# Optimization experiments

Measured on AMD Instinct MI355X. Metric: run time of the kernel, lower is better.

The kernel has to match this reference:

```python
import jax, jax.numpy as jnp
import numpy as np
from jax import lax

# dims (match init_kwargs / input_specs)
B, CIN, H, W = 32, 32, 48, 160
CL = 32            # out_lstm (per-direction hidden channels)
CO = 64            # out_channels of conv
KH, KW, STRIDE = 2, 2, 2
EPS = 1e-5         # BatchNorm2d eps


def setup_inputs() -> dict:
    key = jax.random.key(0)
    ks = jax.random.split(key, 9)
    s = 0.1
    return {
        "x": jax.random.normal(ks[0], (B, CIN, H, W), jnp.float32),
        # per-direction MDLSTM weights: input proj, left-hidden, top-hidden, bias
        "Wx": jax.random.normal(ks[1], (4, CIN, 5 * CL), jnp.float32) * s,
        "Ul": jax.random.normal(ks[2], (4, CL, 5 * CL), jnp.float32) * s,
        "Ut": jax.random.normal(ks[3], (4, CL, 5 * CL), jnp.float32) * s,
        "bias": jnp.zeros((4, 5 * CL), jnp.float32),
        # conv_0 (the original forward uses conv_0 for all four directions)
        "conv_w": jax.random.normal(ks[4], (CO, CL, KH, KW), jnp.float32) * s,
        "conv_b": jnp.zeros((CO,), jnp.float32),
        # BatchNorm2d affine params (training-mode batch statistics)
        "gamma": jnp.ones((CO,), jnp.float32),
        "beta": jnp.zeros((CO,), jnp.float32),
    }


def _mdlstm_dir(xz, Ul, Ut):
    """One scan direction of a Graves-style 2D MDLSTM.
    xz: [H, W, B, 5C] precomputed input projection (incl. bias).
    Gates order: i, f_left, f_top, o, g. Returns h: [H, W, B, C]."""
    C = Ul.shape[0]
    Bn = xz.shape[2]
    zero_row = jnp.zeros((xz.shape[1], Bn, C), xz.dtype)  # [W, B, C]

    def col_step(carry, inp):
        h_l, c_l = carry                 # [B, C] state from the left
        z_c, h_t, c_t = inp              # per-cell input proj + top state
        z = z_c + h_l @ Ul + h_t @ Ut    # [B, 5C]
        i, fl, ft, o, g = jnp.split(z, 5, axis=-1)
        c = (jax.nn.sigmoid(fl) * c_l + jax.nn.sigmoid(ft) * c_t
             + jax.nn.sigmoid(i) * jnp.tanh(g))
        h = jax.nn.sigmoid(o) * jnp.tanh(c)
        return (h, c), (h, c)

    def row_step(carry, xz_row):
        h_top, c_top = carry             # [W, B, C] previous row states
        init = (jnp.zeros((Bn, C), xz.dtype), jnp.zeros((Bn, C), xz.dtype))
        _, (h_row, c_row) = lax.scan(col_step, init, (xz_row, h_top, c_top))
        return (h_row, c_row), h_row

    _, h_all = lax.scan(row_step, (zero_row, zero_row), xz)  # [H, W, B, C]
    return h_all


def reference(x, Wx, Ul, Ut, bias, conv_w, conv_b, gamma, beta):
    xh = jnp.transpose(x, (2, 3, 0, 1))  # [H, W, B, Cin]
    dirs = []
    for d in range(4):  # 4 scan directions: flip combinations of H / W
        xd = xh
        if d in (1, 3):
            xd = xd[:, ::-1]
        if d in (2, 3):
            xd = xd[::-1]
        # big upfront GEMM: input projection for every cell
        xz = jnp.einsum('hwbc,cd->hwbd', xd, Wx[d]) + bias[d]
        h = _mdlstm_dir(xz, Ul[d], Ut[d])
        if d in (2, 3):
            h = h[::-1]
        if d in (1, 3):
            h = h[:, ::-1]
        dirs.append(h)
    # original applies conv_0 to each direction then sums; conv is linear so
    # conv0(x0)+conv0(x1)+conv0(x2)+conv0(x3) == conv0(x0+x1+x2+x3) + 4*bias
    hsum = dirs[0] + dirs[1] + dirs[2] + dirs[3]           # [H, W, B, C]
    hsum = jnp.transpose(hsum, (2, 3, 0, 1))               # [B, C, H, W]
    y = lax.conv_general_dilated(hsum, conv_w, (STRIDE, STRIDE), 'VALID',
                                 dimension_numbers=('NCHW', 'OIHW', 'NCHW'))
    y = y + (4.0 * conv_b)[None, :, None, None]
    y = jnp.tanh(y)
    # BatchNorm2d, training mode (biased batch variance, eps=1e-5)
    mean = y.mean(axis=(0, 2, 3), keepdims=True)
    var = jnp.square(y - mean).mean(axis=(0, 2, 3), keepdims=True)
    yn = (y - mean) * lax.rsqrt(var + EPS)
    return gamma[None, :, None, None] * yn + beta[None, :, None, None]
```

## Files before the change

### kernel.cpp

```cpp
#include <hip/hip_runtime.h>

typedef __bf16 bf16;
typedef __bf16 bf16x8 __attribute__((ext_vector_type(8)));
typedef float  f32x4  __attribute__((ext_vector_type(4)));
typedef int    i32x2  __attribute__((ext_vector_type(2)));
typedef unsigned long long u64;

#define HH 48
#define WW 160
#define BB 32
#define CINC 32
#define CLC 32
#define COC 64
#define OHH 24
#define OWW 80
#define RD 8
#define SLOT_U64 1280

__device__ __forceinline__ bool probe_bf16(const void* gamma) {
  return ((const unsigned short*)gamma)[0] == 0x3F80;
}
__device__ __forceinline__ float rd_in(const void* p, int idx, bool isb) {
  return isb ? (float)((const bf16*)p)[idx] : ((const float*)p)[idx];
}
__device__ __forceinline__ float fsig(float x) {
  return 1.0f / (1.0f + __expf(-x));
}
__device__ __forceinline__ float ftanh(float x) {
  return 1.0f - 2.0f / (1.0f + __expf(2.0f * x));
}

union PK64 { bf16 h[4]; u64 q; };
union FRU { f32x4 f; bf16x8 v; };

__global__ __launch_bounds__(256) void k_params(const void* __restrict__ bias,
                                                const void* __restrict__ conv_w,
                                                const void* __restrict__ conv_b,
                                                const void* __restrict__ gamma,
                                                const void* __restrict__ beta,
                                                float* __restrict__ biasf,
                                                float* __restrict__ convwT,
                                                float* __restrict__ convbf,
                                                float* __restrict__ gammaf,
                                                float* __restrict__ betaf) {
  bool isb = probe_bf16(gamma);
  int i = blockIdx.x * 256 + threadIdx.x;
  if (i < 640)  biasf[i]  = rd_in(bias, i, isb);
  if (i < 8192) {
    int kk = i >> 11, co = (i >> 5) & 63, cl = i & 31;
    convwT[i] = rd_in(conv_w, co * 128 + cl * 4 + kk, isb);
  }
  if (i < 64) {
    convbf[i] = rd_in(conv_b, i, isb);
    gammaf[i] = rd_in(gamma, i, isb);
    betaf[i]  = rd_in(beta, i, isb);
  }
}

__global__ __launch_bounds__(256) void k_transpose3(const void* __restrict__ x,
                                                    const void* __restrict__ gamma,
                                                    bf16* __restrict__ xT3) {
  bool isb = probe_bf16(gamma);
  int h  = blockIdx.x / 20;
  int w0 = (blockIdx.x % 20) * 8;
  __shared__ float tile[BB * CINC * 8];
  for (int e = threadIdx.x; e < BB * CINC * 8; e += 256) {
    int dw = e & 7, c = (e >> 3) & 31, b = e >> 8;
    tile[e] = rd_in(x, ((b * CINC + c) * HH + h) * WW + w0 + dw, isb);
  }
  __syncthreads();
  const size_t PL = (size_t)HH * WW * 1024;
  for (int e = threadIdx.x; e < BB * CINC * 8; e += 256) {
    int c = e & 31, b = (e >> 5) & 31, dw = e >> 10;
    float v = tile[(b * 32 + c) * 8 + dw];
    bf16 p0 = (bf16)v; float r = v - (float)p0;
    bf16 p1 = (bf16)r;
    bf16 p2 = (bf16)(r - (float)p1);
    size_t base = ((size_t)h * WW + w0 + dw) * 1024 + b * 32 + c;
    xT3[base] = p0; xT3[PL + base] = p1; xT3[2 * PL + base] = p2;
  }
}

#define MF5(Aop, PB, KS)                                                       \
  { _Pragma("unroll") for (int g = 0; g < 5; g++)                              \
      acc[g] = __builtin_amdgcn_mfma_f32_16x16x32_bf16(Aop, Ufr[PB][KS][g],    \
                                                       acc[g], 0, 0, 0); }

__global__ __launch_bounds__(256, 1) void k_mdlstm(
    const bf16* __restrict__ xT3,
    const void* __restrict__ Wx, const void* __restrict__ Ul,
    const void* __restrict__ Ut, const void* __restrict__ gamma_raw,
    const float* __restrict__ biasf,
    u64* __restrict__ ring,
    int* __restrict__ flags,
    int* __restrict__ cons,
    float* __restrict__ planes) {
  bool isb = probe_bf16(gamma_raw);
  int d = blockIdx.x / 48, i = blockIdx.x % 48;
  int fi = d * 48 + i;
  int gh = (d & 2) ? (HH - 1 - i) : i;
  int tid = threadIdx.x;
  int lane = tid & 63, wv = tid >> 6;
  int mtile = wv & 1, hf = wv >> 1, nsub = hf * 16;
  int l15 = lane & 15, quad = lane >> 4;
  int m = mtile * 16 + l15;
  int cl  = nsub + l15;
  int b0q = mtile * 16 + quad * 4;
  int rb = lane & 3;
  int bC = b0q + rb;
  int cl0C = nsub + (l15 & 12);

  __shared__ bf16 Ust[160 * 96];
  __shared__ __align__(16) bf16 Afr[2][3][1024];

  bf16x8 Ufr[3][3][5];
  for (int q = 0; q < 3; q++) {
    for (int e = tid; e < 160 * 96; e += 256) {
      int n = e / 96, k = e % 96;
      float v;
      if (k < 32)      v = rd_in(Ul, (d * 32 + k) * 160 + n, isb);
      else if (k < 64) v = rd_in(Ut, (d * 32 + (k - 32)) * 160 + n, isb);
      else             v = rd_in(Wx, (d * 32 + (k - 64)) * 160 + n, isb);
      bf16 p0 = (bf16)v; float r = v - (float)p0;
      bf16 p1 = (bf16)r;
      Ust[e] = (q == 0) ? p0 : (q == 1) ? p1 : (bf16)(r - (float)p1);
    }
    __syncthreads();
#pragma unroll
    for (int ks = 0; ks < 3; ks++)
#pragma unroll
      for (int g = 0; g < 5; g++)
        Ufr[q][ks][g] =
            *(const bf16x8*)(&Ust[(nsub + 32 * g + l15) * 96 + ks * 32 + quad * 8]);
    __syncthreads();
  }
  float bi[5];
#pragma unroll
  for (int g = 0; g < 5; g++) bi[g] = biasf[d * 160 + 32 * g + nsub + l15];
  for (int e = tid; e < 2 * 3 * 1024; e += 256) (&Afr[0][0][0])[e] = (bf16)0.f;
  __syncthreads();

  float creg[4] = {0.f, 0.f, 0.f, 0.f};

  int fprev = (i > 0)  ? fi - 1 : fi;
  int fnext = (i < 47) ? fi + 1 : fi;
  int* fdst = flags + ((fi << 5) + (mtile << 1) + hf);
  const int* fsrc = flags + ((fprev << 5) + (mtile << 1));
  int* cdst = cons + ((fi << 5) + (mtile << 1) + hf);
  const int* csrc = cons + ((fnext << 5) + (mtile << 1));
  int flag_known = (i > 0) ? -1 : 0x7FFFFFFF;
  int cons_known = -1;
  i32x2 pf; pf.x = -1; pf.y = -1;

  const int a_rd = m * 64 + ((quad * 16) ^ ((m & 6) << 3));
  const int a_wr = bC * 64 + ((cl0C * 2) ^ ((bC & 6) << 3));

  bf16x8 xreg[3];
  {
    int gw0 = (d & 1) ? (WW - 1) : 0;
#pragma unroll
    for (int p = 0; p < 3; p++)
      xreg[p] = *(const bf16x8*)(xT3 + (size_t)(p * HH + gh) * WW * 1024 +
                                 (size_t)gw0 * 1024 + m * 32 + quad * 8);
  }

  for (int j = 0; j < WW; j++) {
    int gw = (d & 1) ? (WW - 1 - j) : j;

    asm volatile("s_waitcnt vmcnt(0)" : "+v"(pf) :: "memory");
    __builtin_amdgcn_sched_barrier(0);

    if (i < 47 && j > 0 && lane == 0) {
      int fv = j - 1;
      asm volatile("global_store_dword %0, %1, off sc0 sc1"
                   :: "v"(fdst), "v"(fv) : "memory");
    }

    if (i < 47 && j - cons_known > RD) {
      for (;;) {
        i32x2 cv;
        asm volatile("global_load_dwordx2 %0, %1, off sc0 sc1\n\t"
                     "s_waitcnt vmcnt(0)"
                     : "=v"(cv) : "v"(csrc) : "memory");
        cons_known = cv.x < cv.y ? cv.x : cv.y;
        if (j - cons_known <= RD) break;
        __builtin_amdgcn_s_sleep(1);
      }
    }

    if (i > 0 && flag_known < j) {
      flag_known = pf.x < pf.y ? pf.x : pf.y;
      while (flag_known < j) {
        i32x2 fv2;
        asm volatile("global_load_dwordx2 %0, %1, off sc0 sc1\n\t"
                     "s_waitcnt vmcnt(0)"
                     : "=v"(fv2) : "v"(fsrc) : "memory");
        flag_known = fv2.x < fv2.y ? fv2.x : fv2.y;
        if (flag_known < j) __builtin_amdgcn_s_sleep(1);
      }
    }

    FRU ht0, ht1, ht2, ctq;
    if (i > 0) {
      const char* sb =
          (const char*)(ring + (size_t)((fi - 1) * RD + (j & (RD - 1))) * SLOT_U64);
      const void* a0 = sb + 0 * 2048 + m * 64 + quad * 16;
      const void* a1 = sb + 1 * 2048 + m * 64 + quad * 16;
      const void* a2 = sb + 2 * 2048 + m * 64 + quad * 16;
      const void* a3 = sb + 6144 + (size_t)(cl * 32 + b0q) * 4;
      asm volatile(
          "global_load_dwordx4 %0, %4, off sc0 sc1\n\t"
          "global_load_dwordx4 %1, %5, off sc0 sc1\n\t"
          "global_load_dwordx4 %2, %6, off sc0 sc1\n\t"
          "global_load_dwordx4 %3, %7, off sc0 sc1"
          : "=&v"(ht0.f), "=&v"(ht1.f), "=&v"(ht2.f), "=&v"(ctq.f)
          : "v"(a0), "v"(a1), "v"(a2), "v"(a3)
          : "memory");
    } else {
      ht0.f = ht1.f = ht2.f = ctq.f = (f32x4){0.f, 0.f, 0.f, 0.f};
    }

    const int rbuf = (j + 1) & 1;
    bf16x8 Al[3];
#pragma unroll
    for (int p = 0; p < 3; p++)
      Al[p] = *(const bf16x8*)((const char*)&Afr[rbuf][p][0] + a_rd);

    f32x4 acc[5];
#pragma unroll
    for (int g = 0; g < 5; g++) acc[g] = (f32x4){0.f, 0.f, 0.f, 0.f};
    MF5(Al[0], 0, 0) MF5(Al[0], 1, 0) MF5(Al[1], 0, 0)
    MF5(Al[1], 1, 0) MF5(Al[0], 2, 0) MF5(Al[2], 0, 0)
    MF5(xreg[0], 0, 2) MF5(xreg[0], 1, 2) MF5(xreg[1], 0, 2)
    MF5(xreg[1], 1, 2) MF5(xreg[0], 2, 2) MF5(xreg[2], 0, 2)

    if (i > 0)
      asm volatile("s_waitcnt vmcnt(0)"
                   : "+v"(ht0.f), "+v"(ht1.f), "+v"(ht2.f), "+v"(ctq.f)
                   :: "memory");

    MF5(ht0.v, 0, 1) MF5(ht0.v, 1, 1) MF5(ht1.v, 0, 1)
    MF5(ht1.v, 1, 1) MF5(ht0.v, 2, 1) MF5(ht2.v, 0, 1)

    if (i > 0 && (j & 3) == 3 && lane == 0)
      asm volatile("global_store_dword %0, %1, off sc0 sc1"
                   :: "v"(cdst), "v"(j) : "memory");

    if (j + 1 < WW) {
      int gwn = (d & 1) ? (WW - 2 - j) : (j + 1);
#pragma unroll
      for (int p = 0; p < 3; p++)
        xreg[p] = *(const bf16x8*)(xT3 + (size_t)(p * HH + gh) * WW * 1024 +
                                   (size_t)gwn * 1024 + m * 32 + quad * 8);
    }
    if (i > 0)
      asm volatile("global_load_dwordx2 %0, %1, off sc0 sc1"
                   : "=v"(pf) : "v"(fsrc) : "memory");

    PK64 myp[3];
#pragma unroll
    for (int r = 0; r < 4; r++) {
      float zi  = acc[0][r] + bi[0];
      float zfl = acc[1][r] + bi[1];
      float zft = acc[2][r] + bi[2];
      float zo  = acc[3][r] + bi[3];
      float zg  = acc[4][r] + bi[4];
      float cv  = fsig(zfl) * creg[r] + fsig(zft) * ctq.f[r] + fsig(zi) * ftanh(zg);
      float hv  = fsig(zo) * ftanh(cv);
      creg[r] = cv;
      bf16 q0 = (bf16)hv; float r1 = hv - (float)q0;
      bf16 q1 = (bf16)r1;
      bf16 q2 = (bf16)(r1 - (float)q1);
      myp[0].h[r] = q0; myp[1].h[r] = q1; myp[2].h[r] = q2;
    }

    int srcb = lane & ~3;
    PK64 outp[3];
#pragma unroll
    for (int p = 0; p < 3; p++) {
      PK64 o;
#pragma unroll
      for (int c = 0; c < 4; c++) {
        PK64 t; t.q = __shfl(myp[p].q, srcb + c, 64);
        o.h[c] = t.h[rb];
      }
      outp[p] = o;
    }

    if (i < 47) {
      u64* slotw = ring + (size_t)(fi * RD + (j & (RD - 1))) * SLOT_U64;
#pragma unroll
      for (int p = 0; p < 3; p++) {
        u64* ha = &slotw[p * 256 + bC * 8 + (cl0C >> 2)];
        asm volatile("global_store_dwordx2 %0, %1, off sc0 sc1"
                     :: "v"(ha), "v"(outp[p].q) : "memory");
      }
      f32x4 cst;
      cst[0] = creg[0]; cst[1] = creg[1]; cst[2] = creg[2]; cst[3] = creg[3];
      u64* ca = &slotw[768 + ((cl * 32 + b0q) >> 1)];
      asm volatile("global_store_dwordx4 %0, %1, off sc0 sc1"
                   :: "v"(ca), "v"(cst) : "memory");
    }

    {
      f32x4 hp;
#pragma unroll
      for (int c = 0; c < 4; c++)
        hp[c] = (float)outp[0].h[c] + (float)outp[1].h[c] + (float)outp[2].h[c];
      *(f32x4*)(planes + (size_t)((d * HH + gh) * WW + gw) * 1024 + bC * 32 + cl0C) = hp;
    }

#pragma unroll
    for (int p = 0; p < 3; p++)
      *(u64*)((char*)&Afr[j & 1][p][0] + a_wr) = outp[p].q;

    asm volatile("s_waitcnt lgkmcnt(0)" ::: "memory");
    __builtin_amdgcn_s_barrier();
    __builtin_amdgcn_sched_barrier(0);
    asm volatile("" ::: "memory");
  }

  asm volatile("s_waitcnt vmcnt(0)" ::: "memory");
  if (i < 47 && lane == 0) {
    int fv = WW - 1;
    asm volatile("global_store_dword %0, %1, off sc0 sc1"
                 :: "v"(fdst), "v"(fv) : "memory");
  }
}

__global__ __launch_bounds__(256) void k_conv(const float* __restrict__ planes,
                                              const float* __restrict__ convwT,
                                              const float* __restrict__ convbf,
                                              float* __restrict__ y,
                                              float* __restrict__ sums) {
  int b  = blockIdx.x / OHH;
  int oh = blockIdx.x % OHH;
  __shared__ float hs[2 * WW * 36];
  int tid = threadIdx.x;
  int co = tid >> 2, q = tid & 3;

  f32x4 w4[2][2][8];
#pragma unroll
  for (int kh = 0; kh < 2; kh++)
#pragma unroll
    for (int kw = 0; kw < 2; kw++)
#pragma unroll
      for (int c4 = 0; c4 < 8; c4++)
        w4[kh][kw][c4] =
            *(const f32x4*)(&convwT[(((kh * 2 + kw) * 64 + co) * 32) + 4 * c4]);

  for (int e = tid; e < 2 * WW * CLC; e += 256) {
    int kh = e / (WW * CLC);
    int rem = e % (WW * CLC);
    int w = rem >> 5, cl = rem & 31;
    int h = 2 * oh + kh;
    float v = 0.f;
#pragma unroll
    for (int dd = 0; dd < 4; dd++)
      v += planes[(size_t)((dd * HH + h) * WW + w) * 1024 + b * 32 + cl];
    hs[(kh * WW + w) * 36 + cl] = v;
  }
  __syncthreads();

  float bco = 4.f * convbf[co];
  float s = 0.f, s2 = 0.f;
  for (int mm = 0; mm < 20; mm++) {
    int ow = q + 4 * mm;
    float acc = bco;
#pragma unroll
    for (int kh = 0; kh < 2; kh++)
#pragma unroll
      for (int kw = 0; kw < 2; kw++) {
        const float* hp = &hs[(kh * WW + 2 * ow + kw) * 36];
#pragma unroll
        for (int c4 = 0; c4 < 8; c4++) {
          f32x4 h4 = *(const f32x4*)(hp + 4 * c4);
          acc = fmaf(h4[0], w4[kh][kw][c4][0], acc);
          acc = fmaf(h4[1], w4[kh][kw][c4][1], acc);
          acc = fmaf(h4[2], w4[kh][kw][c4][2], acc);
          acc = fmaf(h4[3], w4[kh][kw][c4][3], acc);
        }
      }
    float v = tanhf(acc);
    y[((b * COC + co) * OHH + oh) * OWW + ow] = v;
    s += v; s2 += v * v;
  }
  s  += __shfl_xor(s, 1);  s  += __shfl_xor(s, 2);
  s2 += __shfl_xor(s2, 1); s2 += __shfl_xor(s2, 2);
  if (q == 0) {
    atomicAdd(&sums[co], s);
    atomicAdd(&sums[64 + co], s2);
  }
}

__global__ __launch_bounds__(256) void k_norm(const float* __restrict__ y,
                                              const float* __restrict__ sums,
                                              const float* __restrict__ gammaf,
                                              const float* __restrict__ betaf,
                                              const void* __restrict__ gamma_raw,
                                              void* __restrict__ out) {
  bool isb = probe_bf16(gamma_raw);
  int e = blockIdx.x * 256 + threadIdx.x;
  int co = (e / (OHH * OWW)) & 63;
  const float inv = 1.0f / (32.0f * OHH * OWW);
  float mean = sums[co] * inv;
  float var  = sums[64 + co] * inv - mean * mean;
  float v = (y[e] - mean) * rsqrtf(var + 1e-5f);
  float r = gammaf[co] * v + betaf[co];
  if (isb) ((bf16*)out)[e] = (bf16)r;
  else     ((float*)out)[e] = r;
}

extern "C" void kernel_launch(void* const* d_in, const int* in_sizes, int n_in,
                              void* d_out, int out_size, void* d_ws, size_t ws_size,
                              hipStream_t stream) {
  const void* x      = d_in[0];
  const void* Wx     = d_in[1];
  const void* Ul     = d_in[2];
  const void* Ut     = d_in[3];
  const void* bias   = d_in[4];
  const void* conv_w = d_in[5];
  const void* conv_b = d_in[6];
  const void* gamma  = d_in[7];
  const void* beta   = d_in[8];

  char* ws = (char*)d_ws;
  bf16*  xT3    = (bf16*)(ws);
  u64*   ring   = (u64*)(ws + 47185920);
  float* y      = (float*)(ws + 47185920);
  float* planes = (float*)(ws + 62914560);
  float* sums   = (float*)(ws + 188743680);
  float* biasf  = (float*)(ws + 188744192);
  float* convwT = (float*)(ws + 188746752);
  float* convbf = (float*)(ws + 188779520);
  float* gammaf = (float*)(ws + 188779776);
  float* betaf  = (float*)(ws + 188780032);
  int*   flags  = (int*)  (ws + 188780288);
  int*   cons   = (int*)  (ws + 188804864);

  hipMemsetAsync(sums, 0, 512, stream);
  hipMemsetAsync(flags, 0xFF, 49152, stream);

  k_params<<<32, 256, 0, stream>>>(bias, conv_w, conv_b, gamma, beta,
                                   biasf, convwT, convbf, gammaf, betaf);
  k_transpose3<<<960, 256, 0, stream>>>(x, gamma, xT3);

  k_mdlstm<<<192, 256, 0, stream>>>(xT3, Wx, Ul, Ut, gamma, biasf,
                                    ring, flags, cons, planes);

  k_conv<<<BB * OHH, 256, 0, stream>>>(planes, convwT, convbf, y, sums);
  k_norm<<<3932160 / 256, 256, 0, stream>>>(y, sums, gammaf, betaf, gamma, d_out);
}
```

Baseline: 895.5 us.

## Publish row-ready flag same step and prefetch consumer progress asynchronously

The producer flag for row j is now stored right after the ring slot writes in the same iteration, behind a vmcnt(0) wait, instead of being deferred to the start of the next iteration. This shortens the critical-path latency between a row and the row below it in the wavefront. Consumer-progress flags are now prefetched asynchronously each step instead of polled with a blocking load, and known values are kept monotonic. The cost is an extra full memory wait per step before the flag store, which could serialize outstanding stores.

```diff
diff --git a/kernel.cpp b/kernel.cpp
--- a/kernel.cpp
+++ b/kernel.cpp
@@ -150,7 +150,8 @@
   const int* csrc = cons + ((fnext << 5) + (mtile << 1));
   int flag_known = (i > 0) ? -1 : 0x7FFFFFFF;
   int cons_known = -1;
-  i32x2 pf; pf.x = -1; pf.y = -1;
+  i32x2 pf;  pf.x = -1;  pf.y = -1;
+  i32x2 cpf; cpf.x = -1; cpf.y = -1;
 
   const int a_rd = m * 64 + ((quad * 16) ^ ((m & 6) << 3));
   const int a_wr = bC * 64 + ((cl0C * 2) ^ ((bC & 6) << 3));
@@ -167,35 +168,35 @@
   for (int j = 0; j < WW; j++) {
     int gw = (d & 1) ? (WW - 1 - j) : j;
 
-    asm volatile("s_waitcnt vmcnt(0)" : "+v"(pf) :: "memory");
+    asm volatile("s_waitcnt vmcnt(0)" : "+v"(pf), "+v"(cpf) :: "memory");
     __builtin_amdgcn_sched_barrier(0);
 
-    if (i < 47 && j > 0 && lane == 0) {
-      int fv = j - 1;
-      asm volatile("global_store_dword %0, %1, off sc0 sc1"
-                   :: "v"(fdst), "v"(fv) : "memory");
-    }
-
-    if (i < 47 && j - cons_known > RD) {
-      for (;;) {
-        i32x2 cv;
-        asm volatile("global_load_dwordx2 %0, %1, off sc0 sc1\n\t"
-                     "s_waitcnt vmcnt(0)"
-                     : "=v"(cv) : "v"(csrc) : "memory");
-        cons_known = cv.x < cv.y ? cv.x : cv.y;
-        if (j - cons_known <= RD) break;
-        __builtin_amdgcn_s_sleep(1);
-      }
-    }
-
+    if (i < 47) {
+      int ck = cpf.x < cpf.y ? cpf.x : cpf.y;
+      if (ck > cons_known) cons_known = ck;
+      if (j - cons_known > RD) {
+        for (;;) {
+          i32x2 cv;
+          asm volatile("global_load_dwordx2 %0, %1, off sc0 sc1\n\t"
+                       "s_waitcnt vmcnt(0)"
+                       : "=v"(cv) : "v"(csrc) : "memory");
+          int c2 = cv.x < cv.y ? cv.x : cv.y;
+          if (c2 > cons_known) cons_known = c2;
+          if (j - cons_known <= RD) break;
+          __builtin_amdgcn_s_sleep(1);
+        }
+      }
+    }
     if (i > 0 && flag_known < j) {
-      flag_known = pf.x < pf.y ? pf.x : pf.y;
+      int fk = pf.x < pf.y ? pf.x : pf.y;
+      if (fk > flag_known) flag_known = fk;
       while (flag_known < j) {
         i32x2 fv2;
         asm volatile("global_load_dwordx2 %0, %1, off sc0 sc1\n\t"
                      "s_waitcnt vmcnt(0)"
                      : "=v"(fv2) : "v"(fsrc) : "memory");
-        flag_known = fv2.x < fv2.y ? fv2.x : fv2.y;
+        int f2 = fv2.x < fv2.y ? fv2.x : fv2.y;
+        if (f2 > flag_known) flag_known = f2;
         if (flag_known < j) __builtin_amdgcn_s_sleep(1);
       }
     }
@@ -242,21 +243,6 @@
     MF5(ht0.v, 0, 1) MF5(ht0.v, 1, 1) MF5(ht1.v, 0, 1)
     MF5(ht1.v, 1, 1) MF5(ht0.v, 2, 1) MF5(ht2.v, 0, 1)
 
-    if (i > 0 && (j & 3) == 3 && lane == 0)
-      asm volatile("global_store_dword %0, %1, off sc0 sc1"
-                   :: "v"(cdst), "v"(j) : "memory");
-
-    if (j + 1 < WW) {
-      int gwn = (d & 1) ? (WW - 2 - j) : (j + 1);
-#pragma unroll
-      for (int p = 0; p < 3; p++)
-        xreg[p] = *(const bf16x8*)(xT3 + (size_t)(p * HH + gh) * WW * 1024 +
-                                   (size_t)gwn * 1024 + m * 32 + quad * 8);
-    }
-    if (i > 0)
-      asm volatile("global_load_dwordx2 %0, %1, off sc0 sc1"
-                   : "=v"(pf) : "v"(fsrc) : "memory");
-
     PK64 myp[3];
 #pragma unroll
     for (int r = 0; r < 4; r++) {
@@ -281,8 +267,8 @@
       PK64 o;
 #pragma unroll
       for (int c = 0; c < 4; c++) {
-        PK64 t; t.q = __shfl(myp[p].q, srcb + c, 64);
-        o.h[c] = t.h[rb];
+        PK64 t2; t2.q = __shfl(myp[p].q, srcb + c, 64);
+        o.h[c] = t2.h[rb];
       }
       outp[p] = o;
     }
@@ -300,7 +286,16 @@
       u64* ca = &slotw[768 + ((cl * 32 + b0q) >> 1)];
       asm volatile("global_store_dwordx4 %0, %1, off sc0 sc1"
                    :: "v"(ca), "v"(cst) : "memory");
-    }
+      asm volatile("s_waitcnt vmcnt(0)" ::: "memory");
+      if (lane == 0) {
+        int fv = j;
+        asm volatile("global_store_dword %0, %1, off sc0 sc1"
+                     :: "v"(fdst), "v"(fv) : "memory");
+      }
+    }
+    if (i > 0 && (j & 3) == 3 && lane == 0)
+      asm volatile("global_store_dword %0, %1, off sc0 sc1"
+                   :: "v"(cdst), "v"(j) : "memory");
 
     {
       f32x4 hp;
@@ -309,6 +304,19 @@
         hp[c] = (float)outp[0].h[c] + (float)outp[1].h[c] + (float)outp[2].h[c];
       *(f32x4*)(planes + (size_t)((d * HH + gh) * WW + gw) * 1024 + bC * 32 + cl0C) = hp;
     }
+    if (j + 1 < WW) {
+      int gwn = (d & 1) ? (WW - 2 - j) : (j + 1);
+#pragma unroll
+      for (int p = 0; p < 3; p++)
+        xreg[p] = *(const bf16x8*)(xT3 + (size_t)(p * HH + gh) * WW * 1024 +
+                                   (size_t)gwn * 1024 + m * 32 + quad * 8);
+    }
+    if (i > 0)
+      asm volatile("global_load_dwordx2 %0, %1, off sc0 sc1"
+                   : "=v"(pf) : "v"(fsrc) : "memory");
+    if (i < 47)
+      asm volatile("global_load_dwordx2 %0, %1, off sc0 sc1"
+                   : "=v"(cpf) : "v"(csrc) : "memory");
 
 #pragma unroll
     for (int p = 0; p < 3; p++)
@@ -321,11 +329,6 @@
   }
 
   asm volatile("s_waitcnt vmcnt(0)" ::: "memory");
-  if (i < 47 && lane == 0) {
-    int fv = WW - 1;
-    asm volatile("global_store_dword %0, %1, off sc0 sc1"
-                 :: "v"(fdst), "v"(fv) : "memory");
-  }
 }
 
 __global__ __launch_bounds__(256) void k_conv(const float* __restrict__ planes,
```

Measured after the change: 867.2 us. 3.2% less time.
